# Kernel tuning notes

Measured on AMD Instinct MI355X. Metric: run time of the kernel, lower is better.

Reference implementation:

```python
import jax, jax.numpy as jnp
import numpy as np

D_MODEL = 1024
N_HEADS = 16
D_K = D_MODEL // N_HEADS


def setup_inputs() -> dict:
    key = jax.random.key(0)
    ks = jax.random.split(key, 9)
    s = 1.0 / np.sqrt(D_MODEL)
    inp = {
        'x': jax.random.normal(ks[0], (2, 2048, D_MODEL), dtype=jnp.float32),
        'wq': jax.random.normal(ks[1], (D_MODEL, D_MODEL), dtype=jnp.float32) * s,
        'bq': jnp.zeros((D_MODEL,), dtype=jnp.float32),
        'wk': jax.random.normal(ks[2], (D_MODEL, D_MODEL), dtype=jnp.float32) * s,
        'bk': jnp.zeros((D_MODEL,), dtype=jnp.float32),
        'wv': jax.random.normal(ks[3], (D_MODEL, D_MODEL), dtype=jnp.float32) * s,
        'bv': jnp.zeros((D_MODEL,), dtype=jnp.float32),
        'wo': jax.random.normal(ks[4], (D_MODEL, D_MODEL), dtype=jnp.float32) * s,
        'bo': jnp.zeros((D_MODEL,), dtype=jnp.float32),
    }
    return inp


def _rope_tables(seq_len, dim, dtype):
    inv_freq = 1.0 / (10000.0 ** (jnp.arange(0, dim, 2, dtype=jnp.float32) / dim))
    t = jnp.arange(seq_len, dtype=jnp.float32)
    freqs = jnp.einsum('i,j->ij', t, inv_freq)          # [S, dim/2]
    emb = jnp.concatenate([freqs, freqs], axis=-1)       # [S, dim]
    return jnp.cos(emb).astype(dtype), jnp.sin(emb).astype(dtype)


def _rotate_half(x):
    half = x.shape[-1] // 2
    return jnp.concatenate([-x[..., half:], x[..., :half]], axis=-1)


def reference(x, wq, bq, wk, bk, wv, bv, wo, bo):
    B, S, _ = x.shape
    H, Dk = N_HEADS, D_K
    # QKV projections (torch Linear: x @ W^T + b)
    q = (x @ wq.T + bq).reshape(B, S, H, Dk).transpose(0, 2, 1, 3)  # [B,H,S,Dk]
    k = (x @ wk.T + bk).reshape(B, S, H, Dk).transpose(0, 2, 1, 3)
    v = (x @ wv.T + bv).reshape(B, S, H, Dk).transpose(0, 2, 1, 3)
    # RoPE
    cos, sin = _rope_tables(S, Dk, x.dtype)  # [S, Dk] each
    q = q * cos + _rotate_half(q) * sin
    k = k * cos + _rotate_half(k) * sin
    # scaled dot-product attention (full scores, softmax over keys)
    scores = jnp.einsum('bhqd,bhkd->bhqk', q, k) / jnp.sqrt(jnp.asarray(Dk, x.dtype))
    attn = jax.nn.softmax(scores, axis=-1)
    out = jnp.einsum('bhqk,bhkd->bqhd', attn, v).reshape(B, S, H * Dk)
    return out @ wo.T + bo
```

## Files before the change

kernel.cpp:

```cpp
#include <hip/hip_runtime.h>
#include <stdint.h>


typedef __attribute__((ext_vector_type(8))) __bf16 bf16x8;
typedef __attribute__((ext_vector_type(4))) short short4v;
typedef __attribute__((ext_vector_type(4))) unsigned short ushort4v;
typedef __attribute__((ext_vector_type(2))) unsigned uint2v;
typedef __attribute__((ext_vector_type(4))) float f32x4;

#define GLDS(gp, lp)                                                          \
  __builtin_amdgcn_global_load_lds(                                           \
      (const __attribute__((address_space(1))) void*)(gp),                    \
      (__attribute__((address_space(3))) void*)(lp), 16, 0, 0)

__device__ __forceinline__ unsigned short f2bf(float f) {
  unsigned u = __float_as_uint(f);
  return (unsigned short)((u + 0x7fffu + ((u >> 16) & 1u)) >> 16);
}
__device__ __forceinline__ short4v cvtpk4(float a, float b, float c, float d) {
  unsigned lo, hi;
  asm("v_cvt_pk_bf16_f32 %0, %1, %2" : "=v"(lo) : "v"(a), "v"(b));
  asm("v_cvt_pk_bf16_f32 %0, %1, %2" : "=v"(hi) : "v"(c), "v"(d));
  uint2v u = {lo, hi};
  return __builtin_bit_cast(short4v, u);
}

__global__ __launch_bounds__(256) void cvt_all_k(
    const float* __restrict__ x, const float* __restrict__ wq,
    const float* __restrict__ wk, const float* __restrict__ wv,
    const float* __restrict__ wo, unsigned short* __restrict__ xb,
    unsigned short* __restrict__ wqb, unsigned short* __restrict__ wkb,
    unsigned short* __restrict__ wvb, unsigned short* __restrict__ wob,
    float* __restrict__ cosT, float* __restrict__ sinT) {
  if (blockIdx.x >= 8192) {
    const int idx = (blockIdx.x - 8192) * 256 + threadIdx.x;
    const int s = idx >> 5, i = idx & 31;
    const float freq =
        (float)s * exp2f(-(float)i * (13.287712379549449f / 32.0f));
    cosT[idx] = cosf(freq);
    sinT[idx] = sinf(freq);
    return;
  }
  const long i = (long)(blockIdx.x * 256 + threadIdx.x) * 4;
  const float* src;
  unsigned short* dst;
  long off;
  if (i < 4194304L) {
    src = x; dst = xb; off = i;
  } else {
    long j = i - 4194304L;
    int w = (int)(j >> 20);
    off = j & 1048575L;
    src = (w == 0) ? wq : (w == 1) ? wk : (w == 2) ? wv : wo;
    dst = (w == 0) ? wqb : (w == 1) ? wkb : (w == 2) ? wvb : wob;
  }
  f32x4 v = *(const f32x4*)(src + off);
  ushort4v o;
  o[0] = f2bf(v[0]); o[1] = f2bf(v[1]); o[2] = f2bf(v[2]); o[3] = f2bf(v[3]);
  *(ushort4v*)(dst + off) = o;
}

__device__ __forceinline__ void gemm_core(const unsigned short* __restrict__ A,
                                          const unsigned short* __restrict__ W,
                                          unsigned short* As, unsigned short* Bs,
                                          int rowBase, int colBase,
                                          f32x4 acc[4][4]) {
  const int lane = threadIdx.x & 63, wid = threadIdx.x >> 6;
  const int wr = wid >> 1, wc = wid & 1;
  const int lr = lane >> 3, l8 = lane & 7;
  const int swz = (l8 ^ lr) * 8;
  const int c16 = lane & 15, g = lane >> 4;

  const f32x4 zero = {0.f, 0.f, 0.f, 0.f};
#pragma unroll
  for (int mf = 0; mf < 4; ++mf)
#pragma unroll
    for (int nf = 0; nf < 4; ++nf) acc[mf][nf] = zero;

  for (int kt = 0; kt < 16; ++kt) {
    __syncthreads();
#pragma unroll
    for (int c2 = 0; c2 < 4; ++c2) {
      const int cc = wid * 4 + c2;
      const int r = cc * 8 + lr;
      GLDS(A + (size_t)(rowBase + r) * 1024 + kt * 64 + swz, As + cc * 512);
      GLDS(W + (size_t)(colBase + r) * 1024 + kt * 64 + swz, Bs + cc * 512);
    }
    __syncthreads();
#pragma unroll
    for (int ks = 0; ks < 2; ++ks) {
      bf16x8 af[4], bfr[4];
#pragma unroll
      for (int mf = 0; mf < 4; ++mf) {
        const int r = wr * 64 + mf * 16 + c16;
        const int kb = (g * 16 + ks * 64) ^ ((r & 7) * 16);
        af[mf] = *(const bf16x8*)((const char*)As + r * 128 + kb);
      }
#pragma unroll
      for (int nf = 0; nf < 4; ++nf) {
        const int r = wc * 64 + nf * 16 + c16;
        const int kb = (g * 16 + ks * 64) ^ ((r & 7) * 16);
        bfr[nf] = *(const bf16x8*)((const char*)Bs + r * 128 + kb);
      }
#pragma unroll
      for (int mf = 0; mf < 4; ++mf)
#pragma unroll
        for (int nf = 0; nf < 4; ++nf)
          acc[mf][nf] = __builtin_amdgcn_mfma_f32_16x16x32_bf16(
              af[mf], bfr[nf], acc[mf][nf], 0, 0, 0);
    }
  }
}

__global__ __launch_bounds__(256) void qkv_gemm_k(
    const unsigned short* __restrict__ xb, const unsigned short* __restrict__ wqb,
    const unsigned short* __restrict__ wkb, const unsigned short* __restrict__ wvb,
    const float* __restrict__ bq, const float* __restrict__ bk,
    const float* __restrict__ bv, const float* __restrict__ cosT,
    const float* __restrict__ sinT, unsigned short* __restrict__ Qr,
    unsigned short* __restrict__ Kr, unsigned short* __restrict__ Vt) {
  __shared__ unsigned short As[8192], Bs[8192];
  const int z = blockIdx.z;
  const unsigned short* W = (z == 0) ? wqb : (z == 1) ? wkb : wvb;
  const float* bias = (z == 0) ? bq : (z == 1) ? bk : bv;
  const int rowBase = blockIdx.x * 128, colBase = blockIdx.y * 128;
  f32x4 acc[4][4];
  gemm_core(xb, W, As, Bs, rowBase, colBase, acc);

  const int lane = threadIdx.x & 63, wid = threadIdx.x >> 6;
  const int wr = wid >> 1, wc = wid & 1, c16 = lane & 15, g = lane >> 4;
  if (z <= 1) {
    unsigned short* dst = z ? Kr : Qr;
    const float SC = z ? 1.0f : 0.125f * 1.44269504088896f;
    const int h = blockIdx.y * 2 + wc;
    const float bb0 = bias[colBase + wc * 64 + 0 * 16 + c16];
    const float bb1 = bias[colBase + wc * 64 + 1 * 16 + c16];
    const float bb2 = bias[colBase + wc * 64 + 2 * 16 + c16];
    const float bb3 = bias[colBase + wc * 64 + 3 * 16 + c16];
#pragma unroll
    for (int mf = 0; mf < 4; ++mf) {
      const int n0 = rowBase + wr * 64 + mf * 16 + g * 4;
#pragma unroll
      for (int reg = 0; reg < 4; ++reg) {
        const int n = n0 + reg;
        const int b = n >> 11, s = n & 2047;
        const float c0 = cosT[(s << 5) + c16], s0 = sinT[(s << 5) + c16];
        const float c1 = cosT[(s << 5) + c16 + 16],
                    s1 = sinT[(s << 5) + c16 + 16];
        const float a0 = acc[mf][0][reg] + bb0;
        const float a1 = acc[mf][1][reg] + bb1;
        const float a2 = acc[mf][2][reg] + bb2;
        const float a3 = acc[mf][3][reg] + bb3;
        unsigned short* dp =
            dst + (size_t)((b * 16 + h) * 2048 + s) * 64 + c16;
        dp[0] = f2bf((a0 * c0 - a2 * s0) * SC);
        dp[16] = f2bf((a1 * c1 - a3 * s1) * SC);
        dp[32] = f2bf((a2 * c0 + a0 * s0) * SC);
        dp[48] = f2bf((a3 * c1 + a1 * s1) * SC);
      }
    }
  } else {
#pragma unroll
    for (int nf = 0; nf < 4; ++nf) {
      const int col = colBase + wc * 64 + nf * 16 + c16;
      const float bb = bias[col];
#pragma unroll
      for (int mf = 0; mf < 4; ++mf) {
        const int n0 = rowBase + wr * 64 + mf * 16 + g * 4;
        const int btc = n0 >> 11, s0 = n0 & 2047;
        ushort4v pk;
#pragma unroll
        for (int reg = 0; reg < 4; ++reg) pk[reg] = f2bf(acc[mf][nf][reg] + bb);
        *(ushort4v*)(Vt + ((size_t)(btc * 1024 + col)) * 2048 + s0) = pk;
      }
    }
  }
}

__global__ __launch_bounds__(256) void out_gemm_k(
    const unsigned short* __restrict__ attn, const unsigned short* __restrict__ wob,
    const float* __restrict__ bo, float* __restrict__ out) {
  __shared__ unsigned short As[8192], Bs[8192];
  const int rowBase = blockIdx.x * 128, colBase = blockIdx.y * 128;
  f32x4 acc[4][4];
  gemm_core(attn, wob, As, Bs, rowBase, colBase, acc);

  const int lane = threadIdx.x & 63, wid = threadIdx.x >> 6;
  const int wr = wid >> 1, wc = wid & 1, c16 = lane & 15, g = lane >> 4;
#pragma unroll
  for (int nf = 0; nf < 4; ++nf) {
    const int col = colBase + wc * 64 + nf * 16 + c16;
    const float bb = bo[col];
#pragma unroll
    for (int mf = 0; mf < 4; ++mf) {
      const int r0 = rowBase + wr * 64 + mf * 16 + g * 4;
#pragma unroll
      for (int reg = 0; reg < 4; ++reg)
        out[(size_t)(r0 + reg) * 1024 + col] = acc[mf][nf][reg] + bb;
    }
  }
}

__global__ __launch_bounds__(512) void attn_k(
    const unsigned short* __restrict__ Qr, const unsigned short* __restrict__ Kr,
    const unsigned short* __restrict__ Vt, unsigned short* __restrict__ attn) {
  __shared__ unsigned short Ks[3][4096], Vs[3][4096];
  const int lane = threadIdx.x & 63, w = threadIdx.x >> 6;
  const int bh = blockIdx.x, qt = blockIdx.y;
  const int c = lane & 15, g = lane >> 4;
  const int l3 = lane >> 3, l7 = lane & 7;
  const int swz8 = (l7 ^ l3) * 8;
  const unsigned short* Qh = Qr + (size_t)bh * 2048 * 64;
  const unsigned short* Kh = Kr + (size_t)bh * 2048 * 64;
  const unsigned short* Vh = Vt + (size_t)bh * 64 * 2048;
  const int qbase = qt * 256 + w * 32;

  const bf16x8 qa0 = *(const bf16x8*)(Qh + (size_t)(qbase + c) * 64 + g * 8);
  const bf16x8 qa1 =
      *(const bf16x8*)(Qh + (size_t)(qbase + c) * 64 + g * 8 + 32);
  const bf16x8 qb0 =
      *(const bf16x8*)(Qh + (size_t)(qbase + 16 + c) * 64 + g * 8);
  const bf16x8 qb1 =
      *(const bf16x8*)(Qh + (size_t)(qbase + 16 + c) * 64 + g * 8 + 32);

  f32x4 oa[4], ob[4];
#pragma unroll
  for (int b2 = 0; b2 < 4; ++b2) {
    oa[b2] = (f32x4){0.f, 0.f, 0.f, 0.f};
    ob[b2] = (f32x4){0.f, 0.f, 0.f, 0.f};
  }
  f32x4 oea = {0.f, 0.f, 0.f, 0.f}, oeb = oea;
  const short4v ones = {0x3F80, 0x3F80, 0x3F80, 0x3F80};
  const f32x4 cinit = {-12.f, -12.f, -12.f, -12.f};

#define STAGE(ktile, buf)                                                     \
  do {                                                                        \
    char* KsB_ = (char*)&Ks[buf][0];                                          \
    char* VsB_ = (char*)&Vs[buf][0];                                          \
    _Pragma("unroll") for (int j = 0; j < 2; ++j) {                           \
      const int ch = w * 2 + j;                                               \
      if (ch < 8) {                                                           \
        GLDS(Kh + (size_t)((ktile)*64 + ch * 8 + l3) * 64 + swz8,             \
             KsB_ + ch * 1024);                                               \
      } else {                                                                \
        const int cv = ch - 8;                                                \
        GLDS(Vh + (size_t)(cv * 8 + l3) * 2048 + (ktile)*64 + swz8,           \
             VsB_ + cv * 1024);                                               \
      }                                                                       \
    }                                                                         \
  } while (0)

  STAGE(0, 0);
  STAGE(1, 1);
  asm volatile("s_waitcnt vmcnt(2)" ::: "memory");
  __syncthreads();
  int bc = 0, bs = 2;

  for (int kt = 0; kt < 32; ++kt) {
    if (kt < 30) STAGE(kt + 2, bs);
    const char* KsB = (const char*)&Ks[bc][0];
    const char* VsB = (const char*)&Vs[bc][0];

    f32x4 sa[4], sb[4];
    __builtin_amdgcn_s_setprio(1);
#pragma unroll
    for (int kk = 0; kk < 4; ++kk) {
      const int r = kk * 16 + c;
      const bf16x8 kf0 =
          *(const bf16x8*)(KsB + r * 128 + ((g * 16) ^ ((c & 7) * 16)));
      const bf16x8 kf1 =
          *(const bf16x8*)(KsB + r * 128 + ((64 + g * 16) ^ ((c & 7) * 16)));
      f32x4 t = __builtin_amdgcn_mfma_f32_16x16x32_bf16(kf0, qa0, cinit, 0, 0, 0);
      sa[kk] = __builtin_amdgcn_mfma_f32_16x16x32_bf16(kf1, qa1, t, 0, 0, 0);
      f32x4 u = __builtin_amdgcn_mfma_f32_16x16x32_bf16(kf0, qb0, cinit, 0, 0, 0);
      sb[kk] = __builtin_amdgcn_mfma_f32_16x16x32_bf16(kf1, qb1, u, 0, 0, 0);
    }
    __builtin_amdgcn_s_setprio(0);

    short4v pba[4], pbb[4];
#pragma unroll
    for (int kk = 0; kk < 4; ++kk) {
      pba[kk] = cvtpk4(__builtin_amdgcn_exp2f(sa[kk][0]),
                       __builtin_amdgcn_exp2f(sa[kk][1]),
                       __builtin_amdgcn_exp2f(sa[kk][2]),
                       __builtin_amdgcn_exp2f(sa[kk][3]));
      pbb[kk] = cvtpk4(__builtin_amdgcn_exp2f(sb[kk][0]),
                       __builtin_amdgcn_exp2f(sb[kk][1]),
                       __builtin_amdgcn_exp2f(sb[kk][2]),
                       __builtin_amdgcn_exp2f(sb[kk][3]));
    }

    __builtin_amdgcn_s_setprio(1);
#pragma unroll
    for (int kk = 0; kk < 4; ++kk) {
#pragma unroll
      for (int b2 = 0; b2 < 4; ++b2) {
        const int vd = b2 * 16 + c;
        const short4v vf = *(const short4v*)(
            VsB + vd * 128 + ((kk * 32 + g * 8) ^ ((c & 7) * 16)));
        oa[b2] = __builtin_amdgcn_mfma_f32_16x16x16bf16_1k(vf, pba[kk], oa[b2],
                                                           0, 0, 0);
        ob[b2] = __builtin_amdgcn_mfma_f32_16x16x16bf16_1k(vf, pbb[kk], ob[b2],
                                                           0, 0, 0);
      }
      oea = __builtin_amdgcn_mfma_f32_16x16x16bf16_1k(ones, pba[kk], oea, 0, 0, 0);
      oeb = __builtin_amdgcn_mfma_f32_16x16x16bf16_1k(ones, pbb[kk], oeb, 0, 0, 0);
    }
    __builtin_amdgcn_s_setprio(0);

    if (kt < 31) {
      if (kt < 30) {
        asm volatile("s_waitcnt vmcnt(2)" ::: "memory");
      } else {
        asm volatile("s_waitcnt vmcnt(0)" ::: "memory");
      }
      __syncthreads();
    }
    bc = (bc == 2) ? 0 : bc + 1;
    bs = (bs == 2) ? 0 : bs + 1;
  }

  const float inva = 1.0f / oea[0];
  const float invb = 1.0f / oeb[0];
  const int b = bh >> 4, h = bh & 15;
  const int na = b * 2048 + qbase + c;
  unsigned short* opa = attn + (size_t)na * 1024 + h * 64;
  unsigned short* opb = opa + (size_t)16 * 1024;
#pragma unroll
  for (int b2 = 0; b2 < 4; ++b2) {
    ushort4v st;
    st[0] = f2bf(oa[b2][0] * inva);
    st[1] = f2bf(oa[b2][1] * inva);
    st[2] = f2bf(oa[b2][2] * inva);
    st[3] = f2bf(oa[b2][3] * inva);
    *(ushort4v*)(opa + b2 * 16 + g * 4) = st;
    ushort4v su;
    su[0] = f2bf(ob[b2][0] * invb);
    su[1] = f2bf(ob[b2][1] * invb);
    su[2] = f2bf(ob[b2][2] * invb);
    su[3] = f2bf(ob[b2][3] * invb);
    *(ushort4v*)(opb + b2 * 16 + g * 4) = su;
  }
}

extern "C" void kernel_launch(void* const* d_in, const int* in_sizes, int n_in,
                              void* d_out, int out_size, void* d_ws,
                              size_t ws_size, hipStream_t stream) {
  const float* x = (const float*)d_in[0];
  const float* wq = (const float*)d_in[1];
  const float* bq = (const float*)d_in[2];
  const float* wk = (const float*)d_in[3];
  const float* bk = (const float*)d_in[4];
  const float* wv = (const float*)d_in[5];
  const float* bv = (const float*)d_in[6];
  const float* wo = (const float*)d_in[7];
  const float* bo = (const float*)d_in[8];
  float* out = (float*)d_out;

  unsigned short* xb = (unsigned short*)d_ws;
  unsigned short* wqb = xb + 4194304;
  unsigned short* wkb = wqb + 1048576;
  unsigned short* wvb = wkb + 1048576;
  unsigned short* wob = wvb + 1048576;
  unsigned short* Qr = wob + 1048576;
  unsigned short* Kr = Qr + 4194304;
  unsigned short* Vt = Kr + 4194304;
  unsigned short* attnb = Vt + 4194304;
  float* cosT = (float*)(attnb + 4194304);
  float* sinT = cosT + 65536;

  cvt_all_k<<<dim3(8448), 256, 0, stream>>>(x, wq, wk, wv, wo, xb, wqb, wkb,
                                            wvb, wob, cosT, sinT);
  qkv_gemm_k<<<dim3(32, 8, 3), 256, 0, stream>>>(xb, wqb, wkb, wvb, bq, bk, bv,
                                                 cosT, sinT, Qr, Kr, Vt);
  attn_k<<<dim3(32, 8), 512, 0, stream>>>(Qr, Kr, Vt, attnb);
  out_gemm_k<<<dim3(32, 8), 256, 0, stream>>>(attnb, wob, bo, out);
}
```

Measured before the change: 122.9 us.

## Triple-buffer GEMM LDS tiles with K=32 stages and async prefetch

The shared GEMM core used by the QKV and output projections now uses three LDS buffers of 32-wide K tiles and prefetches two stages ahead with global_load_lds. Explicit vmcnt waits replace the old load-then-sync pattern, so MFMA work can overlap global loads. The LDS swizzle is redesigned for 64-byte rows. In exchange there are twice as many k-iterations, each with a barrier, and slightly more LDS per block (48KB against 32KB), which may lower occupancy.

```diff
diff --git a/kernel.cpp b/kernel.cpp
--- a/kernel.cpp
+++ b/kernel.cpp
@@ -67,9 +67,10 @@
                                           f32x4 acc[4][4]) {
   const int lane = threadIdx.x & 63, wid = threadIdx.x >> 6;
   const int wr = wid >> 1, wc = wid & 1;
-  const int lr = lane >> 3, l8 = lane & 7;
-  const int swz = (l8 ^ lr) * 8;
   const int c16 = lane & 15, g = lane >> 4;
+  const int rc = lane >> 2;
+  const int srcslot = (lane & 3) ^ ((lane >> 2) & 3) ^ ((lane >> 4) & 3);
+  const int rdswz = ((g ^ (c16 & 3) ^ ((c16 >> 2) & 3)) * 16);
 
   const f32x4 zero = {0.f, 0.f, 0.f, 0.f};
 #pragma unroll
@@ -77,39 +78,58 @@
 #pragma unroll
     for (int nf = 0; nf < 4; ++nf) acc[mf][nf] = zero;
 
-  for (int kt = 0; kt < 16; ++kt) {
-    __syncthreads();
-#pragma unroll
-    for (int c2 = 0; c2 < 4; ++c2) {
-      const int cc = wid * 4 + c2;
-      const int r = cc * 8 + lr;
-      GLDS(A + (size_t)(rowBase + r) * 1024 + kt * 64 + swz, As + cc * 512);
-      GLDS(W + (size_t)(colBase + r) * 1024 + kt * 64 + swz, Bs + cc * 512);
-    }
-    __syncthreads();
-#pragma unroll
-    for (int ks = 0; ks < 2; ++ks) {
-      bf16x8 af[4], bfr[4];
-#pragma unroll
-      for (int mf = 0; mf < 4; ++mf) {
-        const int r = wr * 64 + mf * 16 + c16;
-        const int kb = (g * 16 + ks * 64) ^ ((r & 7) * 16);
-        af[mf] = *(const bf16x8*)((const char*)As + r * 128 + kb);
-      }
-#pragma unroll
-      for (int nf = 0; nf < 4; ++nf) {
-        const int r = wc * 64 + nf * 16 + c16;
-        const int kb = (g * 16 + ks * 64) ^ ((r & 7) * 16);
-        bfr[nf] = *(const bf16x8*)((const char*)Bs + r * 128 + kb);
-      }
-#pragma unroll
-      for (int mf = 0; mf < 4; ++mf)
-#pragma unroll
-        for (int nf = 0; nf < 4; ++nf)
-          acc[mf][nf] = __builtin_amdgcn_mfma_f32_16x16x32_bf16(
-              af[mf], bfr[nf], acc[mf][nf], 0, 0, 0);
-    }
-  }
+#define GSTAGE(ktile, buf)                                                    \
+  do {                                                                        \
+    _Pragma("unroll") for (int c2 = 0; c2 < 4; ++c2) {                        \
+      const int ch = wid * 4 + c2;                                            \
+      if (ch < 8) {                                                           \
+        GLDS(A + (size_t)(rowBase + ch * 16 + rc) * 1024 + (ktile)*32 +       \
+                 srcslot * 8,                                                 \
+             As + (buf)*4096 + ch * 512);                                     \
+      } else {                                                                \
+        const int cb = ch - 8;                                                \
+        GLDS(W + (size_t)(colBase + cb * 16 + rc) * 1024 + (ktile)*32 +       \
+                 srcslot * 8,                                                 \
+             Bs + (buf)*4096 + cb * 512);                                     \
+      }                                                                       \
+    }                                                                         \
+  } while (0)
+
+  GSTAGE(0, 0);
+  GSTAGE(1, 1);
+  asm volatile("s_waitcnt vmcnt(4)" ::: "memory");
+  __syncthreads();
+  int bc = 0, bs = 2;
+
+  for (int kt = 0; kt < 32; ++kt) {
+    if (kt < 30) GSTAGE(kt + 2, bs);
+    const char* AsB = (const char*)As + bc * 8192;
+    const char* BsB = (const char*)Bs + bc * 8192;
+    bf16x8 af[4], bfr[4];
+#pragma unroll
+    for (int mf = 0; mf < 4; ++mf)
+      af[mf] = *(const bf16x8*)(AsB + (wr * 64 + mf * 16 + c16) * 64 + rdswz);
+#pragma unroll
+    for (int nf = 0; nf < 4; ++nf)
+      bfr[nf] = *(const bf16x8*)(BsB + (wc * 64 + nf * 16 + c16) * 64 + rdswz);
+#pragma unroll
+    for (int mf = 0; mf < 4; ++mf)
+#pragma unroll
+      for (int nf = 0; nf < 4; ++nf)
+        acc[mf][nf] = __builtin_amdgcn_mfma_f32_16x16x32_bf16(
+            af[mf], bfr[nf], acc[mf][nf], 0, 0, 0);
+    if (kt < 31) {
+      if (kt < 30) {
+        asm volatile("s_waitcnt vmcnt(4)" ::: "memory");
+      } else {
+        asm volatile("s_waitcnt vmcnt(0)" ::: "memory");
+      }
+      __syncthreads();
+    }
+    bc = (bc == 2) ? 0 : bc + 1;
+    bs = (bs == 2) ? 0 : bs + 1;
+  }
+#undef GSTAGE
 }
 
 __global__ __launch_bounds__(256) void qkv_gemm_k(
@@ -119,13 +139,13 @@
     const float* __restrict__ bv, const float* __restrict__ cosT,
     const float* __restrict__ sinT, unsigned short* __restrict__ Qr,
     unsigned short* __restrict__ Kr, unsigned short* __restrict__ Vt) {
-  __shared__ unsigned short As[8192], Bs[8192];
+  __shared__ unsigned short As[3][4096], Bs[3][4096];
   const int z = blockIdx.z;
   const unsigned short* W = (z == 0) ? wqb : (z == 1) ? wkb : wvb;
   const float* bias = (z == 0) ? bq : (z == 1) ? bk : bv;
   const int rowBase = blockIdx.x * 128, colBase = blockIdx.y * 128;
   f32x4 acc[4][4];
-  gemm_core(xb, W, As, Bs, rowBase, colBase, acc);
+  gemm_core(xb, W, &As[0][0], &Bs[0][0], rowBase, colBase, acc);
 
   const int lane = threadIdx.x & 63, wid = threadIdx.x >> 6;
   const int wr = wid >> 1, wc = wid & 1, c16 = lane & 15, g = lane >> 4;
@@ -180,10 +200,10 @@
 __global__ __launch_bounds__(256) void out_gemm_k(
     const unsigned short* __restrict__ attn, const unsigned short* __restrict__ wob,
     const float* __restrict__ bo, float* __restrict__ out) {
-  __shared__ unsigned short As[8192], Bs[8192];
+  __shared__ unsigned short As[3][4096], Bs[3][4096];
   const int rowBase = blockIdx.x * 128, colBase = blockIdx.y * 128;
   f32x4 acc[4][4];
-  gemm_core(attn, wob, As, Bs, rowBase, colBase, acc);
+  gemm_core(attn, wob, &As[0][0], &Bs[0][0], rowBase, colBase, acc);
 
   const int lane = threadIdx.x & 63, wid = threadIdx.x >> 6;
   const int wr = wid >> 1, wc = wid & 1, c16 = lane & 15, g = lane >> 4;
```

After: 123.7 us. Within noise of the previous version (+0.6%).
